# Optimization experiments

Measured on AMD Instinct MI355X. Metric: run time of the kernel, lower is better.

Reference implementation:

```python
import jax, jax.numpy as jnp
import numpy as np

N_NODES = 100000
N_EDGES = 1600000
IN_C = 128
HID_C = 32
HEADS = 4
OUT_C = 40
N_GRAPHS = 64
NEG_SLOPE = 0.2  # PyG GATConv default


def setup_inputs() -> dict:
    key = jax.random.key(0)
    ks = jax.random.split(key, 12)
    x = jax.random.normal(ks[0], (N_NODES, IN_C), dtype=jnp.float32)
    edge_index = jax.random.randint(ks[1], (2, N_EDGES), 0, N_NODES, dtype=jnp.int64)
    batch = jnp.sort(jax.random.randint(ks[2], (N_NODES,), 0, N_GRAPHS, dtype=jnp.int64))
    s1 = 1.0 / np.sqrt(IN_C)
    s2 = 1.0 / np.sqrt(HEADS * HID_C)
    W1 = jax.random.normal(ks[3], (IN_C, HEADS * HID_C), dtype=jnp.float32) * s1
    a1_src = jax.random.normal(ks[4], (HEADS, HID_C), dtype=jnp.float32) * s1
    a1_dst = jax.random.normal(ks[5], (HEADS, HID_C), dtype=jnp.float32) * s1
    b1 = jnp.zeros((HEADS * HID_C,), dtype=jnp.float32)
    W2 = jax.random.normal(ks[6], (HEADS * HID_C, OUT_C), dtype=jnp.float32) * s2
    a2_src = jax.random.normal(ks[7], (1, OUT_C), dtype=jnp.float32) * s2
    a2_dst = jax.random.normal(ks[8], (1, OUT_C), dtype=jnp.float32) * s2
    b2 = jnp.zeros((OUT_C,), dtype=jnp.float32)
    return {"x": x, "edge_index": edge_index, "batch": batch,
            "W1": W1, "a1_src": a1_src, "a1_dst": a1_dst, "b1": b1,
            "W2": W2, "a2_src": a2_src, "a2_dst": a2_dst, "b2": b2}


def gat_conv(x, src, dst, W, a_src, a_dst, bias, heads, out_c, concat):
    """PyG-style GATConv (eval mode, self-loops included in src/dst)."""
    N = x.shape[0]
    h = (x @ W).reshape(N, heads, out_c)              # [N,H,C]
    alpha_s = jnp.einsum('nhc,hc->nh', h, a_src)      # [N,H]
    alpha_d = jnp.einsum('nhc,hc->nh', h, a_dst)
    e = alpha_s[src] + alpha_d[dst]                   # [E,H]
    e = jnp.where(e > 0, e, NEG_SLOPE * e)            # LeakyReLU(0.2)
    # segment softmax over edges grouped by destination node
    m = jax.ops.segment_max(e, dst, num_segments=N)   # [N,H]
    ex = jnp.exp(e - m[dst])
    denom = jax.ops.segment_sum(ex, dst, num_segments=N)
    alpha = ex / (denom[dst] + 1e-16)                 # [E,H]
    msg = h[src] * alpha[..., None]                   # [E,H,C]
    out = jax.ops.segment_sum(msg, dst, num_segments=N)  # [N,H,C]
    if concat:
        out = out.reshape(N, heads * out_c)
    else:
        out = out.mean(axis=1)
    return out + bias


def reference(x, edge_index, batch, W1, a1_src, a1_dst, b1, W2, a2_src, a2_dst, b2):
    N = x.shape[0]
    # add self-loops (PyG GATConv default add_self_loops=True)
    loop = jnp.arange(N, dtype=edge_index.dtype)
    src = jnp.concatenate([edge_index[0], loop])
    dst = jnp.concatenate([edge_index[1], loop])
    h = gat_conv(x, src, dst, W1, a1_src, a1_dst, b1, HEADS, HID_C, concat=True)
    h = jax.nn.elu(h)
    h = gat_conv(h, src, dst, W2, a2_src, a2_dst, b2, 1, OUT_C, concat=False)
    # global mean pool over graphs
    sums = jax.ops.segment_sum(h, batch, num_segments=N_GRAPHS)
    counts = jax.ops.segment_sum(jnp.ones((N,), dtype=h.dtype), batch, num_segments=N_GRAPHS)
    return sums / jnp.maximum(counts, 1.0)[:, None]
```

## Files before the change

### kernel.cpp

```cpp
#include <hip/hip_runtime.h>

#define NNODES 100000
#define NEDGES 1600000
#define ETOT   1700000
#define NGRAPH 64
#define NEG    0.2f
#define NB_SCAN 98
#define NPART  8
#define DPP    12500
#define SCAT_BPP 128
#define SCAT_CHR 12500
#define DSL    98
#define PCH    1024
#define NGB    1563
#define HB     521
#define HEPB   3072
#define FGRID  2084

using f32x2 = __attribute__((ext_vector_type(2))) float;

__device__ __forceinline__ float f4get(const float4& v, int j) {
    return j == 0 ? v.x : j == 1 ? v.y : j == 2 ? v.z : v.w;
}

__device__ __forceinline__ unsigned short f2bf(float f) {
    unsigned u = __float_as_uint(f);
    u = (u + 0x7fffu + ((u >> 16) & 1u)) >> 16;
    return (unsigned short)u;
}
__device__ __forceinline__ float bf_lo(unsigned u) { return __uint_as_float(u << 16); }
__device__ __forceinline__ float bf_hi(unsigned u) { return __uint_as_float(u & 0xffff0000u); }

__global__ __launch_bounds__(256) void k_init(int* __restrict__ cnt, float* __restrict__ partial) {
    int t = threadIdx.x, b = blockIdx.x;
#pragma unroll
    for (int j = 0; j < 4; ++j) {
        int idx = b * 1024 + t * 4 + j;
        if (idx < NNODES) cnt[idx] = 1;
    }
    int pi = b * 256 + t;
    if (pi < NGRAPH * 40) partial[pi] = 0.f;
}

__global__ __launch_bounds__(256, 4) void k_fused1(const int* __restrict__ ei,
        int* __restrict__ cnt, int* __restrict__ rank,
        const float* __restrict__ x, const float* __restrict__ W1,
        const float* __restrict__ a1s, const float* __restrict__ a1d,
        unsigned* __restrict__ h1q, float* __restrict__ as1, float* __restrict__ ad1) {
    __shared__ float sX[64 * 128];
    int bid = blockIdx.x;
    if ((bid & 3) == 3) {
        int hb = bid >> 2;
        int t = threadIdx.x;
        int e0 = hb * HEPB;
        int e1 = e0 + HEPB; if (e1 > NEDGES) e1 = NEDGES;
        for (int e = e0 + t; e < e1; e += 1024) {
            int eA = e, eB = e + 256, eC = e + 512, eD = e + 768;
            bool vA = eA < e1, vB = eB < e1, vC = eC < e1, vD = eD < e1;
            int dA = 0, dB = 0, dC = 0, dD = 0;
            if (vA) dA = ei[NEDGES + eA];
            if (vB) dB = ei[NEDGES + eB];
            if (vC) dC = ei[NEDGES + eC];
            if (vD) dD = ei[NEDGES + eD];
            int rA = 0, rB = 0, rC = 0, rD = 0;
            if (vA) rA = atomicAdd(&cnt[dA], 1);
            if (vB) rB = atomicAdd(&cnt[dB], 1);
            if (vC) rC = atomicAdd(&cnt[dC], 1);
            if (vD) rD = atomicAdd(&cnt[dD], 1);
            if (vA) rank[eA] = rA;
            if (vB) rank[eB] = rB;
            if (vC) rank[eC] = rC;
            if (vD) rank[eD] = rD;
        }
        return;
    }
    int gb = (bid >> 2) * 3 + (bid & 3);
    if (gb >= NGB) return;
    int t = threadIdx.x;
    int nbase = gb * 64;
    int nrows = NNODES - nbase; if (nrows > 64) nrows = 64;
    {
        const float4* X4 = (const float4*)(x + (size_t)nbase * 128);
        float4* sX4 = (float4*)sX;
        for (int i = t; i < nrows * 32; i += 256) sX4[i] = X4[i];
    }
    __syncthreads();

    int colg = t & 31, rowg = t >> 5;
    int c0 = colg * 4, n0 = rowg * 8;
    float acc[8][4];
#pragma unroll
    for (int i = 0; i < 8; ++i)
        acc[i][0] = acc[i][1] = acc[i][2] = acc[i][3] = 0.f;

    for (int k = 0; k < 128; k += 4) {
        float4 w0 = *(const float4*)&W1[(size_t)(k + 0) * 128 + c0];
        float4 w1 = *(const float4*)&W1[(size_t)(k + 1) * 128 + c0];
        float4 w2 = *(const float4*)&W1[(size_t)(k + 2) * 128 + c0];
        float4 w3 = *(const float4*)&W1[(size_t)(k + 3) * 128 + c0];
#pragma unroll
        for (int i = 0; i < 8; ++i) {
            float4 xv = *(const float4*)&sX[(n0 + i) * 128 + k];
            acc[i][0] = fmaf(xv.x, w0.x, acc[i][0]); acc[i][1] = fmaf(xv.x, w0.y, acc[i][1]);
            acc[i][2] = fmaf(xv.x, w0.z, acc[i][2]); acc[i][3] = fmaf(xv.x, w0.w, acc[i][3]);
            acc[i][0] = fmaf(xv.y, w1.x, acc[i][0]); acc[i][1] = fmaf(xv.y, w1.y, acc[i][1]);
            acc[i][2] = fmaf(xv.y, w1.z, acc[i][2]); acc[i][3] = fmaf(xv.y, w1.w, acc[i][3]);
            acc[i][0] = fmaf(xv.z, w2.x, acc[i][0]); acc[i][1] = fmaf(xv.z, w2.y, acc[i][1]);
            acc[i][2] = fmaf(xv.z, w2.z, acc[i][2]); acc[i][3] = fmaf(xv.z, w2.w, acc[i][3]);
            acc[i][0] = fmaf(xv.w, w3.x, acc[i][0]); acc[i][1] = fmaf(xv.w, w3.y, acc[i][1]);
            acc[i][2] = fmaf(xv.w, w3.z, acc[i][2]); acc[i][3] = fmaf(xv.w, w3.w, acc[i][3]);
        }
    }

    int head = colg >> 3;
    float ws0 = a1s[c0], ws1 = a1s[c0 + 1], ws2 = a1s[c0 + 2], ws3 = a1s[c0 + 3];
    float wd0 = a1d[c0], wd1 = a1d[c0 + 1], wd2 = a1d[c0 + 2], wd3 = a1d[c0 + 3];
#pragma unroll
    for (int i = 0; i < 8; ++i) {
        int n = n0 + i;
        float ps = acc[i][0] * ws0 + acc[i][1] * ws1 + acc[i][2] * ws2 + acc[i][3] * ws3;
        float pd = acc[i][0] * wd0 + acc[i][1] * wd1 + acc[i][2] * wd2 + acc[i][3] * wd3;
        ps += __shfl_xor(ps, 1); ps += __shfl_xor(ps, 2); ps += __shfl_xor(ps, 4);
        pd += __shfl_xor(pd, 1); pd += __shfl_xor(pd, 2); pd += __shfl_xor(pd, 4);
        if (n < nrows) {
            int q = __builtin_amdgcn_cvt_pk_fp8_f32(acc[i][0], acc[i][1], 0, false);
            q = __builtin_amdgcn_cvt_pk_fp8_f32(acc[i][2], acc[i][3], q, true);
            h1q[((size_t)(nbase + n)) * 32 + colg] = (unsigned)q;
            if ((colg & 7) == 0) {
                as1[(size_t)(nbase + n) * 4 + head] = ps;
                ad1[(size_t)(nbase + n) * 4 + head] = pd;
            }
        }
    }
}

__global__ __launch_bounds__(256) void k_scan1(const int* __restrict__ cnt,
                                               int* __restrict__ excl,
                                               int* __restrict__ bsum) {
    __shared__ int tmp[256];
    int t = threadIdx.x;
    int base = blockIdx.x * 1024 + t * 4;
    int v0 = base + 0 < NNODES ? cnt[base + 0] : 0;
    int v1 = base + 1 < NNODES ? cnt[base + 1] : 0;
    int v2 = base + 2 < NNODES ? cnt[base + 2] : 0;
    int v3 = base + 3 < NNODES ? cnt[base + 3] : 0;
    int tot = v0 + v1 + v2 + v3;
    tmp[t] = tot;
    __syncthreads();
    for (int off = 1; off < 256; off <<= 1) {
        int x = (t >= off) ? tmp[t - off] : 0;
        __syncthreads();
        tmp[t] += x;
        __syncthreads();
    }
    int tbase = tmp[t] - tot;
    if (base + 0 < NNODES) excl[base + 0] = tbase;
    if (base + 1 < NNODES) excl[base + 1] = tbase + v0;
    if (base + 2 < NNODES) excl[base + 2] = tbase + v0 + v1;
    if (base + 3 < NNODES) excl[base + 3] = tbase + v0 + v1 + v2;
    if (t == 255) bsum[blockIdx.x] = tmp[255];
}

__global__ __launch_bounds__(256) void k_offs(const int* __restrict__ excl,
                                              const int* __restrict__ bsum,
                                              int* __restrict__ offs) {
    __shared__ int sp;
    int b = blockIdx.x, t = threadIdx.x;
    if (t == 0) {
        int p = 0;
        for (int i = 0; i < b; ++i) p += bsum[i];
        sp = p;
    }
    __syncthreads();
    int prefix = sp;
#pragma unroll
    for (int j = 0; j < 4; ++j) {
        int idx = b * 1024 + t * 4 + j;
        if (idx < NNODES) offs[idx] = excl[idx] + prefix;
    }
}

__global__ __launch_bounds__(256) void k_scatter(const int* __restrict__ ei,
                                                 const int* __restrict__ rank,
                                                 const int* __restrict__ offs,
                                                 int* __restrict__ csr_src) {
    int p = blockIdx.x & (NPART - 1);
    int chunk = blockIdx.x / NPART;
    int dlo = p * DPP, dhi = dlo + DPP;
    {
        int d = dlo + chunk * DSL + threadIdx.x;
        if (threadIdx.x < DSL && d < dhi) csr_src[offs[d]] = d;
    }
    int e0 = chunk * SCAT_CHR;
    int e1 = e0 + SCAT_CHR; if (e1 > NEDGES) e1 = NEDGES;
    for (int e = e0 + threadIdx.x; e < e1; e += 1024) {
        int eA = e, eB = e + 256, eC = e + 512, eD = e + 768;
        bool vA = eA < e1, vB = eB < e1, vC = eC < e1, vD = eD < e1;
        int dA = -1, dB = -1, dC = -1, dD = -1;
        if (vA) dA = ei[NEDGES + eA];
        if (vB) dB = ei[NEDGES + eB];
        if (vC) dC = ei[NEDGES + eC];
        if (vD) dD = ei[NEDGES + eD];
        if (dA >= dlo && dA < dhi) csr_src[offs[dA] + rank[eA]] = ei[eA];
        if (dB >= dlo && dB < dhi) csr_src[offs[dB] + rank[eB]] = ei[eB];
        if (dC >= dlo && dC < dhi) csr_src[offs[dC] + rank[eC]] = ei[eC];
        if (dD >= dlo && dD < dhi) csr_src[offs[dD] + rank[eD]] = ei[eD];
    }
}

__global__ __launch_bounds__(256) void k_node1(const int* __restrict__ csr_src,
        const int* __restrict__ offs, const int* __restrict__ cnt,
        const unsigned* __restrict__ h1q,
        const float4* __restrict__ as1v, const float4* __restrict__ ad1v,
        unsigned* __restrict__ out1b) {
    __shared__ float4 exbuf[8][32];
    int t = threadIdx.x;
    int grp = t >> 5, lane = t & 31;
    int node = blockIdx.x * 8 + grp;
    if (node >= NNODES) return;
    int head = lane >> 3;
    int off = offs[node];
    int deg = cnt[node];
    float4 adv = ad1v[node];
    float4 dp = make_float4(0.f, 0.f, 0.f, 0.f);
    float4 acc = make_float4(0.f, 0.f, 0.f, 0.f);
    const float* exs = (const float*)&exbuf[grp][0];

    for (int base = 0; base < deg; base += 32) {
        int m = deg - base; if (m > 32) m = 32;
        int sv = 0;
        if (lane < m) {
            sv = csr_src[off + base + lane];
            float4 av = as1v[sv];
            float v; float4 e;
            v = av.x + adv.x; v = v > 0.f ? v : NEG * v; e.x = __expf(v);
            v = av.y + adv.y; v = v > 0.f ? v : NEG * v; e.y = __expf(v);
            v = av.z + adv.z; v = v > 0.f ? v : NEG * v; e.z = __expf(v);
            v = av.w + adv.w; v = v > 0.f ? v : NEG * v; e.w = __expf(v);
            exbuf[grp][lane] = e;
            dp.x += e.x; dp.y += e.y; dp.z += e.z; dp.w += e.w;
        }
        __builtin_amdgcn_wave_barrier();
        int i = 0;
        for (; i + 4 <= m; i += 4) {
            int s0 = __shfl(sv, i + 0, 32);
            int s1 = __shfl(sv, i + 1, 32);
            int s2 = __shfl(sv, i + 2, 32);
            int s3 = __shfl(sv, i + 3, 32);
            unsigned q0 = h1q[(size_t)s0 * 32 + lane];
            unsigned q1 = h1q[(size_t)s1 * 32 + lane];
            unsigned q2 = h1q[(size_t)s2 * 32 + lane];
            unsigned q3 = h1q[(size_t)s3 * 32 + lane];
            float a0 = exs[(i + 0) * 4 + head];
            float a1 = exs[(i + 1) * 4 + head];
            float a2 = exs[(i + 2) * 4 + head];
            float a3 = exs[(i + 3) * 4 + head];
            f32x2 lo, hi;
            lo = __builtin_amdgcn_cvt_pk_f32_fp8((int)q0, false);
            hi = __builtin_amdgcn_cvt_pk_f32_fp8((int)q0, true);
            acc.x = fmaf(lo.x, a0, acc.x); acc.y = fmaf(lo.y, a0, acc.y);
            acc.z = fmaf(hi.x, a0, acc.z); acc.w = fmaf(hi.y, a0, acc.w);
            lo = __builtin_amdgcn_cvt_pk_f32_fp8((int)q1, false);
            hi = __builtin_amdgcn_cvt_pk_f32_fp8((int)q1, true);
            acc.x = fmaf(lo.x, a1, acc.x); acc.y = fmaf(lo.y, a1, acc.y);
            acc.z = fmaf(hi.x, a1, acc.z); acc.w = fmaf(hi.y, a1, acc.w);
            lo = __builtin_amdgcn_cvt_pk_f32_fp8((int)q2, false);
            hi = __builtin_amdgcn_cvt_pk_f32_fp8((int)q2, true);
            acc.x = fmaf(lo.x, a2, acc.x); acc.y = fmaf(lo.y, a2, acc.y);
            acc.z = fmaf(hi.x, a2, acc.z); acc.w = fmaf(hi.y, a2, acc.w);
            lo = __builtin_amdgcn_cvt_pk_f32_fp8((int)q3, false);
            hi = __builtin_amdgcn_cvt_pk_f32_fp8((int)q3, true);
            acc.x = fmaf(lo.x, a3, acc.x); acc.y = fmaf(lo.y, a3, acc.y);
            acc.z = fmaf(hi.x, a3, acc.z); acc.w = fmaf(hi.y, a3, acc.w);
        }
        for (; i < m; ++i) {
            int s = __shfl(sv, i, 32);
            float a = exs[i * 4 + head];
            unsigned hq = h1q[(size_t)s * 32 + lane];
            f32x2 lo = __builtin_amdgcn_cvt_pk_f32_fp8((int)hq, false);
            f32x2 hi = __builtin_amdgcn_cvt_pk_f32_fp8((int)hq, true);
            acc.x = fmaf(lo.x, a, acc.x);
            acc.y = fmaf(lo.y, a, acc.y);
            acc.z = fmaf(hi.x, a, acc.z);
            acc.w = fmaf(hi.y, a, acc.w);
        }
        __builtin_amdgcn_wave_barrier();
    }
#pragma unroll
    for (int msk = 1; msk < 32; msk <<= 1) {
        dp.x += __shfl_xor(dp.x, msk, 32);
        dp.y += __shfl_xor(dp.y, msk, 32);
        dp.z += __shfl_xor(dp.z, msk, 32);
        dp.w += __shfl_xor(dp.w, msk, 32);
    }
    float inv = 1.f / f4get(dp, head);
    unsigned p0 = (unsigned)f2bf(acc.x * inv) | ((unsigned)f2bf(acc.y * inv) << 16);
    unsigned p1 = (unsigned)f2bf(acc.z * inv) | ((unsigned)f2bf(acc.w * inv) << 16);
    uint2 pk; pk.x = p0; pk.y = p1;
    *(uint2*)&out1b[(size_t)node * 64 + lane * 2] = pk;
}

__global__ __launch_bounds__(256) void k_gemm2(const unsigned* __restrict__ in_b,
                                               const float* __restrict__ W2,
                                               const float* __restrict__ b1,
                                               const float* __restrict__ a2s,
                                               const float* __restrict__ a2d,
                                               unsigned short* __restrict__ h2b,
                                               float* __restrict__ as2,
                                               float* __restrict__ ad2) {
    __shared__ float sW[128 * 40];
    __shared__ float sX[128 * 132];
    int t = threadIdx.x;
    for (int i = t; i < 128 * 40 / 4; i += 256) ((float4*)sW)[i] = ((const float4*)W2)[i];
    int nbase = blockIdx.x * 128;
    int nrows = NNODES - nbase; if (nrows > 128) nrows = 128;
    {
        const uint4* X4 = (const uint4*)(in_b + (size_t)nbase * 64);
        for (int i = t; i < nrows * 16; i += 256) {
            int row = i >> 4, c8 = i & 15;
            uint4 v = X4[i];
            float4 bb0 = *(const float4*)&b1[c8 * 8];
            float4 bb1 = *(const float4*)&b1[c8 * 8 + 4];
            float f0 = bf_lo(v.x) + bb0.x, f1 = bf_hi(v.x) + bb0.y;
            float f2 = bf_lo(v.y) + bb0.z, f3 = bf_hi(v.y) + bb0.w;
            float f4 = bf_lo(v.z) + bb1.x, f5 = bf_hi(v.z) + bb1.y;
            float f6 = bf_lo(v.w) + bb1.z, f7 = bf_hi(v.w) + bb1.w;
            f0 = f0 > 0.f ? f0 : __expf(f0) - 1.f;
            f1 = f1 > 0.f ? f1 : __expf(f1) - 1.f;
            f2 = f2 > 0.f ? f2 : __expf(f2) - 1.f;
            f3 = f3 > 0.f ? f3 : __expf(f3) - 1.f;
            f4 = f4 > 0.f ? f4 : __expf(f4) - 1.f;
            f5 = f5 > 0.f ? f5 : __expf(f5) - 1.f;
            f6 = f6 > 0.f ? f6 : __expf(f6) - 1.f;
            f7 = f7 > 0.f ? f7 : __expf(f7) - 1.f;
            float* sp = &sX[row * 132 + c8 * 8];
            *(float4*)sp       = make_float4(f0, f1, f2, f3);
            *(float4*)(sp + 4) = make_float4(f4, f5, f6, f7);
        }
    }
    __syncthreads();

    int colg = t & 7, nodeg = t >> 3;
    int c0 = colg * 5;
    float acc[4][5];
#pragma unroll
    for (int i = 0; i < 4; ++i)
#pragma unroll
        for (int c = 0; c < 5; ++c) acc[i][c] = 0.f;

    for (int k = 0; k < 128; k += 4) {
        float4 xv[4];
#pragma unroll
        for (int i = 0; i < 4; ++i)
            xv[i] = *(const float4*)&sX[(nodeg + 32 * i) * 132 + k];
#pragma unroll
        for (int j = 0; j < 4; ++j) {
            float w0 = sW[(k + j) * 40 + c0 + 0];
            float w1 = sW[(k + j) * 40 + c0 + 1];
            float w2 = sW[(k + j) * 40 + c0 + 2];
            float w3 = sW[(k + j) * 40 + c0 + 3];
            float w4 = sW[(k + j) * 40 + c0 + 4];
#pragma unroll
            for (int i = 0; i < 4; ++i) {
                float xs = f4get(xv[i], j);
                acc[i][0] = fmaf(xs, w0, acc[i][0]);
                acc[i][1] = fmaf(xs, w1, acc[i][1]);
                acc[i][2] = fmaf(xs, w2, acc[i][2]);
                acc[i][3] = fmaf(xs, w3, acc[i][3]);
                acc[i][4] = fmaf(xs, w4, acc[i][4]);
            }
        }
    }

    float ws0 = a2s[c0], ws1 = a2s[c0 + 1], ws2 = a2s[c0 + 2], ws3 = a2s[c0 + 3], ws4 = a2s[c0 + 4];
    float wd0 = a2d[c0], wd1 = a2d[c0 + 1], wd2 = a2d[c0 + 2], wd3 = a2d[c0 + 3], wd4 = a2d[c0 + 4];
#pragma unroll
    for (int i = 0; i < 4; ++i) {
        int n = nodeg + 32 * i;
        float ps = acc[i][0]*ws0 + acc[i][1]*ws1 + acc[i][2]*ws2 + acc[i][3]*ws3 + acc[i][4]*ws4;
        float pd = acc[i][0]*wd0 + acc[i][1]*wd1 + acc[i][2]*wd2 + acc[i][3]*wd3 + acc[i][4]*wd4;
        ps += __shfl_xor(ps, 1); ps += __shfl_xor(ps, 2); ps += __shfl_xor(ps, 4);
        pd += __shfl_xor(pd, 1); pd += __shfl_xor(pd, 2); pd += __shfl_xor(pd, 4);
        if (n < nrows) {
            unsigned short* hp = h2b + (size_t)(nbase + n) * 40 + c0;
#pragma unroll
            for (int c = 0; c < 5; ++c) hp[c] = f2bf(acc[i][c]);
            if (colg == 0) {
                as2[nbase + n] = ps;
                ad2[nbase + n] = pd;
            }
        }
    }
}

__global__ __launch_bounds__(256) void k_node2(const int* __restrict__ csr_src,
        const int* __restrict__ offs, const int* __restrict__ cnt,
        const unsigned short* __restrict__ h2b,
        const float* __restrict__ as2, const float* __restrict__ ad2,
        float* __restrict__ out2) {
    int t = threadIdx.x;
    int grp = t >> 4, lane = t & 15;
    int node = blockIdx.x * 16 + grp;
    if (node >= NNODES) return;
    int off = offs[node];
    int deg = cnt[node];
    float adv = ad2[node];
    float dp = 0.f;
    float4 acc = make_float4(0.f, 0.f, 0.f, 0.f);

    for (int base = 0; base < deg; base += 16) {
        int m = deg - base; if (m > 16) m = 16;
        int sv = 0; float ex = 0.f;
        if (lane < m) {
            sv = csr_src[off + base + lane];
            float v = as2[sv] + adv;
            v = v > 0.f ? v : NEG * v;
            ex = __expf(v);
            dp += ex;
        }
        int i = 0;
        for (; i + 4 <= m; i += 4) {
            int s0 = __shfl(sv, i + 0, 16);
            int s1 = __shfl(sv, i + 1, 16);
            int s2 = __shfl(sv, i + 2, 16);
            int s3 = __shfl(sv, i + 3, 16);
            float a0 = __shfl(ex, i + 0, 16);
            float a1 = __shfl(ex, i + 1, 16);
            float a2 = __shfl(ex, i + 2, 16);
            float a3 = __shfl(ex, i + 3, 16);
            if (lane < 10) {
                uint2 h0 = *(const uint2*)(h2b + (size_t)s0 * 40 + lane * 4);
                uint2 h1 = *(const uint2*)(h2b + (size_t)s1 * 40 + lane * 4);
                uint2 h2 = *(const uint2*)(h2b + (size_t)s2 * 40 + lane * 4);
                uint2 h3 = *(const uint2*)(h2b + (size_t)s3 * 40 + lane * 4);
                acc.x = fmaf(bf_lo(h0.x), a0, acc.x); acc.y = fmaf(bf_hi(h0.x), a0, acc.y);
                acc.z = fmaf(bf_lo(h0.y), a0, acc.z); acc.w = fmaf(bf_hi(h0.y), a0, acc.w);
                acc.x = fmaf(bf_lo(h1.x), a1, acc.x); acc.y = fmaf(bf_hi(h1.x), a1, acc.y);
                acc.z = fmaf(bf_lo(h1.y), a1, acc.z); acc.w = fmaf(bf_hi(h1.y), a1, acc.w);
                acc.x = fmaf(bf_lo(h2.x), a2, acc.x); acc.y = fmaf(bf_hi(h2.x), a2, acc.y);
                acc.z = fmaf(bf_lo(h2.y), a2, acc.z); acc.w = fmaf(bf_hi(h2.y), a2, acc.w);
                acc.x = fmaf(bf_lo(h3.x), a3, acc.x); acc.y = fmaf(bf_hi(h3.x), a3, acc.y);
                acc.z = fmaf(bf_lo(h3.y), a3, acc.z); acc.w = fmaf(bf_hi(h3.y), a3, acc.w);
            }
        }
        for (; i < m; ++i) {
            int s = __shfl(sv, i, 16);
            float a = __shfl(ex, i, 16);
            if (lane < 10) {
                uint2 hv = *(const uint2*)(h2b + (size_t)s * 40 + lane * 4);
                acc.x = fmaf(bf_lo(hv.x), a, acc.x);
                acc.y = fmaf(bf_hi(hv.x), a, acc.y);
                acc.z = fmaf(bf_lo(hv.y), a, acc.z);
                acc.w = fmaf(bf_hi(hv.y), a, acc.w);
            }
        }
    }
#pragma unroll
    for (int msk = 1; msk < 16; msk <<= 1) dp += __shfl_xor(dp, msk, 16);
    float inv = 1.f / dp;
    if (lane < 10) {
        float4 o; o.x = acc.x * inv; o.y = acc.y * inv; o.z = acc.z * inv; o.w = acc.w * inv;
        *(float4*)(out2 + (size_t)node * 40 + lane * 4) = o;
    }
}

__global__ __launch_bounds__(256) void k_pool1(const float* __restrict__ out2,
        const int* __restrict__ batch, float* __restrict__ partial) {
    int t = threadIdx.x;
    if (t >= 240) return;
    int r = t / 40, c = t - r * 40;
    int base = blockIdx.x * PCH;
    int end = base + PCH; if (end > NNODES) end = NNODES;
    float sum = 0.f; int gcur = -1;
    for (int n = base + r; n < end; n += 6) {
        int g = batch[n];
        if (g != gcur) {
            if (gcur >= 0) unsafeAtomicAdd(&partial[gcur * 40 + c], sum);
            gcur = g; sum = 0.f;
        }
        sum += out2[(size_t)n * 40 + c];
    }
    if (gcur >= 0) unsafeAtomicAdd(&partial[gcur * 40 + c], sum);
}

__global__ void k_pool2(const float* __restrict__ partial, const int* __restrict__ batch,
                        const float* __restrict__ b2, float* __restrict__ out) {
    int i = blockIdx.x * 256 + threadIdx.x;
    if (i >= NGRAPH * 40) return;
    int g = i / 40, c = i - g * 40;
    int lo, hi;
    { int a = 0, b = NNODES; while (a < b) { int m = (a + b) >> 1; if (batch[m] < g) a = m + 1; else b = m; } lo = a; }
    { int a = lo, b = NNODES; while (a < b) { int m = (a + b) >> 1; if (batch[m] < g + 1) a = m + 1; else b = m; } hi = a; }
    int cntg = hi - lo;
    out[i] = cntg > 0 ? partial[i] / (float)cntg + b2[c] : 0.f;
}

extern "C" void kernel_launch(void* const* d_in, const int* in_sizes, int n_in,
                              void* d_out, int out_size, void* d_ws, size_t ws_size,
                              hipStream_t stream) {
    const float* x    = (const float*)d_in[0];
    const int*   ei   = (const int*)d_in[1];
    const int*   batch= (const int*)d_in[2];
    const float* W1   = (const float*)d_in[3];
    const float* a1s  = (const float*)d_in[4];
    const float* a1d  = (const float*)d_in[5];
    const float* b1   = (const float*)d_in[6];
    const float* W2   = (const float*)d_in[7];
    const float* a2s  = (const float*)d_in[8];
    const float* a2d  = (const float*)d_in[9];
    const float* b2   = (const float*)d_in[10];
    float* out = (float*)d_out;

    int* cnt      = (int*)d_ws;
    float* partial= (float*)(cnt + NNODES);
    int* excl     = (int*)(partial + NGRAPH * 40);
    int* offs     = excl + NNODES;
    int* bsum     = offs + NNODES;
    int* rank     = bsum + 128;
    int* csr      = rank + NEDGES;
    float* as1    = (float*)(csr + ETOT);
    float* ad1    = as1 + (size_t)NNODES * 4;
    unsigned* h1q = (unsigned*)(ad1 + (size_t)NNODES * 4);
    unsigned* out1b = h1q + (size_t)NNODES * 32;
    float* as2    = (float*)(out1b + (size_t)NNODES * 64);
    float* ad2    = as2 + NNODES;
    unsigned short* h2b = (unsigned short*)(ad2 + NNODES);
    float* out2   = (float*)(h2b + (size_t)NNODES * 40);

    k_init<<<NB_SCAN, 256, 0, stream>>>(cnt, partial);

    k_fused1<<<FGRID, 256, 0, stream>>>(ei, cnt, rank, x, W1, a1s, a1d, h1q, as1, ad1);

    k_scan1<<<NB_SCAN, 256, 0, stream>>>(cnt, excl, bsum);
    k_offs<<<NB_SCAN, 256, 0, stream>>>(excl, bsum, offs);
    k_scatter<<<NPART * SCAT_BPP, 256, 0, stream>>>(ei, rank, offs, csr);

    k_node1<<<(NNODES + 7) / 8, 256, 0, stream>>>(csr, offs, cnt, h1q,
                                                  (const float4*)as1, (const float4*)ad1, out1b);

    k_gemm2<<<(NNODES + 127) / 128, 256, 0, stream>>>(out1b, W2, b1, a2s, a2d, h2b, as2, ad2);
    k_node2<<<(NNODES + 15) / 16, 256, 0, stream>>>(csr, offs, cnt, h2b, as2, ad2, out2);

    k_pool1<<<(NNODES + PCH - 1) / PCH, 256, 0, stream>>>(out2, batch, partial);
    k_pool2<<<(NGRAPH * 40 + 255) / 256, 256, 0, stream>>>(partial, batch, b2, out);
}
```

Before: 331.9 us.

## Drop init and offset kernels, fold CSR offsets inline, widen gather unroll

Replaces the count-init kernel with a memset and applies the self-loop +1 wherever counts and ranks are read. Removes the per-node offsets kernel: a single-thread kernel scans the block sums, and the scatter and node kernels compute excl[d] + bsum[d>>10] directly. It also repartitions the scatter into 4 destination ranges with 256 edge chunks, and unrolls the layer-1 neighbour gather by 8 instead of 4. The aim is fewer launches and less offset-array traffic, in exchange for an extra load per offset lookup and a serial single-thread scan.

```diff
diff --git a/kernel.cpp b/kernel.cpp
--- a/kernel.cpp
+++ b/kernel.cpp
@@ -6,10 +6,10 @@
 #define NGRAPH 64
 #define NEG    0.2f
 #define NB_SCAN 98
-#define NPART  8
-#define DPP    12500
-#define SCAT_BPP 128
-#define SCAT_CHR 12500
+#define NPART  4
+#define DPP    25000
+#define SCAT_NCH 256
+#define SCAT_CHR 6250
 #define DSL    98
 #define PCH    1024
 #define NGB    1563
@@ -30,17 +30,6 @@
 }
 __device__ __forceinline__ float bf_lo(unsigned u) { return __uint_as_float(u << 16); }
 __device__ __forceinline__ float bf_hi(unsigned u) { return __uint_as_float(u & 0xffff0000u); }
-
-__global__ __launch_bounds__(256) void k_init(int* __restrict__ cnt, float* __restrict__ partial) {
-    int t = threadIdx.x, b = blockIdx.x;
-#pragma unroll
-    for (int j = 0; j < 4; ++j) {
-        int idx = b * 1024 + t * 4 + j;
-        if (idx < NNODES) cnt[idx] = 1;
-    }
-    int pi = b * 256 + t;
-    if (pi < NGRAPH * 40) partial[pi] = 0.f;
-}
 
 __global__ __launch_bounds__(256, 4) void k_fused1(const int* __restrict__ ei,
         int* __restrict__ cnt, int* __restrict__ rank,
@@ -140,10 +129,10 @@
     __shared__ int tmp[256];
     int t = threadIdx.x;
     int base = blockIdx.x * 1024 + t * 4;
-    int v0 = base + 0 < NNODES ? cnt[base + 0] : 0;
-    int v1 = base + 1 < NNODES ? cnt[base + 1] : 0;
-    int v2 = base + 2 < NNODES ? cnt[base + 2] : 0;
-    int v3 = base + 3 < NNODES ? cnt[base + 3] : 0;
+    int v0 = base + 0 < NNODES ? cnt[base + 0] + 1 : 0;
+    int v1 = base + 1 < NNODES ? cnt[base + 1] + 1 : 0;
+    int v2 = base + 2 < NNODES ? cnt[base + 2] + 1 : 0;
+    int v3 = base + 3 < NNODES ? cnt[base + 3] + 1 : 0;
     int tot = v0 + v1 + v2 + v3;
     tmp[t] = tot;
     __syncthreads();
@@ -161,35 +150,24 @@
     if (t == 255) bsum[blockIdx.x] = tmp[255];
 }
 
-__global__ __launch_bounds__(256) void k_offs(const int* __restrict__ excl,
-                                              const int* __restrict__ bsum,
-                                              int* __restrict__ offs) {
-    __shared__ int sp;
-    int b = blockIdx.x, t = threadIdx.x;
-    if (t == 0) {
-        int p = 0;
-        for (int i = 0; i < b; ++i) p += bsum[i];
-        sp = p;
-    }
-    __syncthreads();
-    int prefix = sp;
-#pragma unroll
-    for (int j = 0; j < 4; ++j) {
-        int idx = b * 1024 + t * 4 + j;
-        if (idx < NNODES) offs[idx] = excl[idx] + prefix;
+__global__ void k_scan2(int* __restrict__ bsum) {
+    if (threadIdx.x == 0 && blockIdx.x == 0) {
+        int acc = 0;
+        for (int i = 0; i < NB_SCAN; ++i) { int v = bsum[i]; bsum[i] = acc; acc += v; }
     }
 }
 
 __global__ __launch_bounds__(256) void k_scatter(const int* __restrict__ ei,
                                                  const int* __restrict__ rank,
-                                                 const int* __restrict__ offs,
+                                                 const int* __restrict__ excl,
+                                                 const int* __restrict__ bsum,
                                                  int* __restrict__ csr_src) {
     int p = blockIdx.x & (NPART - 1);
-    int chunk = blockIdx.x / NPART;
+    int chunk = blockIdx.x >> 2;
     int dlo = p * DPP, dhi = dlo + DPP;
     {
         int d = dlo + chunk * DSL + threadIdx.x;
-        if (threadIdx.x < DSL && d < dhi) csr_src[offs[d]] = d;
+        if (threadIdx.x < DSL && d < dhi) csr_src[excl[d] + bsum[d >> 10]] = d;
     }
     int e0 = chunk * SCAT_CHR;
     int e1 = e0 + SCAT_CHR; if (e1 > NEDGES) e1 = NEDGES;
@@ -201,16 +179,16 @@
         if (vB) dB = ei[NEDGES + eB];
         if (vC) dC = ei[NEDGES + eC];
         if (vD) dD = ei[NEDGES + eD];
-        if (dA >= dlo && dA < dhi) csr_src[offs[dA] + rank[eA]] = ei[eA];
-        if (dB >= dlo && dB < dhi) csr_src[offs[dB] + rank[eB]] = ei[eB];
-        if (dC >= dlo && dC < dhi) csr_src[offs[dC] + rank[eC]] = ei[eC];
-        if (dD >= dlo && dD < dhi) csr_src[offs[dD] + rank[eD]] = ei[eD];
+        if (dA >= dlo && dA < dhi) csr_src[excl[dA] + bsum[dA >> 10] + 1 + rank[eA]] = ei[eA];
+        if (dB >= dlo && dB < dhi) csr_src[excl[dB] + bsum[dB >> 10] + 1 + rank[eB]] = ei[eB];
+        if (dC >= dlo && dC < dhi) csr_src[excl[dC] + bsum[dC >> 10] + 1 + rank[eC]] = ei[eC];
+        if (dD >= dlo && dD < dhi) csr_src[excl[dD] + bsum[dD >> 10] + 1 + rank[eD]] = ei[eD];
     }
 }
 
 __global__ __launch_bounds__(256) void k_node1(const int* __restrict__ csr_src,
-        const int* __restrict__ offs, const int* __restrict__ cnt,
-        const unsigned* __restrict__ h1q,
+        const int* __restrict__ excl, const int* __restrict__ bsum,
+        const int* __restrict__ cnt, const unsigned* __restrict__ h1q,
         const float4* __restrict__ as1v, const float4* __restrict__ ad1v,
         unsigned* __restrict__ out1b) {
     __shared__ float4 exbuf[8][32];
@@ -219,8 +197,8 @@
     int node = blockIdx.x * 8 + grp;
     if (node >= NNODES) return;
     int head = lane >> 3;
-    int off = offs[node];
-    int deg = cnt[node];
+    int off = excl[node] + bsum[node >> 10];
+    int deg = cnt[node] + 1;
     float4 adv = ad1v[node];
     float4 dp = make_float4(0.f, 0.f, 0.f, 0.f);
     float4 acc = make_float4(0.f, 0.f, 0.f, 0.f);
@@ -242,19 +220,31 @@
         }
         __builtin_amdgcn_wave_barrier();
         int i = 0;
-        for (; i + 4 <= m; i += 4) {
+        for (; i + 8 <= m; i += 8) {
             int s0 = __shfl(sv, i + 0, 32);
             int s1 = __shfl(sv, i + 1, 32);
             int s2 = __shfl(sv, i + 2, 32);
             int s3 = __shfl(sv, i + 3, 32);
+            int s4 = __shfl(sv, i + 4, 32);
+            int s5 = __shfl(sv, i + 5, 32);
+            int s6 = __shfl(sv, i + 6, 32);
+            int s7 = __shfl(sv, i + 7, 32);
             unsigned q0 = h1q[(size_t)s0 * 32 + lane];
             unsigned q1 = h1q[(size_t)s1 * 32 + lane];
             unsigned q2 = h1q[(size_t)s2 * 32 + lane];
             unsigned q3 = h1q[(size_t)s3 * 32 + lane];
+            unsigned q4 = h1q[(size_t)s4 * 32 + lane];
+            unsigned q5 = h1q[(size_t)s5 * 32 + lane];
+            unsigned q6 = h1q[(size_t)s6 * 32 + lane];
+            unsigned q7 = h1q[(size_t)s7 * 32 + lane];
             float a0 = exs[(i + 0) * 4 + head];
             float a1 = exs[(i + 1) * 4 + head];
             float a2 = exs[(i + 2) * 4 + head];
             float a3 = exs[(i + 3) * 4 + head];
+            float a4 = exs[(i + 4) * 4 + head];
+            float a5 = exs[(i + 5) * 4 + head];
+            float a6 = exs[(i + 6) * 4 + head];
+            float a7 = exs[(i + 7) * 4 + head];
             f32x2 lo, hi;
             lo = __builtin_amdgcn_cvt_pk_f32_fp8((int)q0, false);
             hi = __builtin_amdgcn_cvt_pk_f32_fp8((int)q0, true);
@@ -272,6 +262,22 @@
             hi = __builtin_amdgcn_cvt_pk_f32_fp8((int)q3, true);
             acc.x = fmaf(lo.x, a3, acc.x); acc.y = fmaf(lo.y, a3, acc.y);
             acc.z = fmaf(hi.x, a3, acc.z); acc.w = fmaf(hi.y, a3, acc.w);
+            lo = __builtin_amdgcn_cvt_pk_f32_fp8((int)q4, false);
+            hi = __builtin_amdgcn_cvt_pk_f32_fp8((int)q4, true);
+            acc.x = fmaf(lo.x, a4, acc.x); acc.y = fmaf(lo.y, a4, acc.y);
+            acc.z = fmaf(hi.x, a4, acc.z); acc.w = fmaf(hi.y, a4, acc.w);
+            lo = __builtin_amdgcn_cvt_pk_f32_fp8((int)q5, false);
+            hi = __builtin_amdgcn_cvt_pk_f32_fp8((int)q5, true);
+            acc.x = fmaf(lo.x, a5, acc.x); acc.y = fmaf(lo.y, a5, acc.y);
+            acc.z = fmaf(hi.x, a5, acc.z); acc.w = fmaf(hi.y, a5, acc.w);
+            lo = __builtin_amdgcn_cvt_pk_f32_fp8((int)q6, false);
+            hi = __builtin_amdgcn_cvt_pk_f32_fp8((int)q6, true);
+            acc.x = fmaf(lo.x, a6, acc.x); acc.y = fmaf(lo.y, a6, acc.y);
+            acc.z = fmaf(hi.x, a6, acc.z); acc.w = fmaf(hi.y, a6, acc.w);
+            lo = __builtin_amdgcn_cvt_pk_f32_fp8((int)q7, false);
+            hi = __builtin_amdgcn_cvt_pk_f32_fp8((int)q7, true);
+            acc.x = fmaf(lo.x, a7, acc.x); acc.y = fmaf(lo.y, a7, acc.y);
+            acc.z = fmaf(hi.x, a7, acc.z); acc.w = fmaf(hi.y, a7, acc.w);
         }
         for (; i < m; ++i) {
             int s = __shfl(sv, i, 32);
@@ -394,16 +400,16 @@
 }
 
 __global__ __launch_bounds__(256) void k_node2(const int* __restrict__ csr_src,
-        const int* __restrict__ offs, const int* __restrict__ cnt,
-        const unsigned short* __restrict__ h2b,
+        const int* __restrict__ excl, const int* __restrict__ bsum,
+        const int* __restrict__ cnt, const unsigned short* __restrict__ h2b,
         const float* __restrict__ as2, const float* __restrict__ ad2,
         float* __restrict__ out2) {
     int t = threadIdx.x;
     int grp = t >> 4, lane = t & 15;
     int node = blockIdx.x * 16 + grp;
     if (node >= NNODES) return;
-    int off = offs[node];
-    int deg = cnt[node];
+    int off = excl[node] + bsum[node >> 10];
+    int deg = cnt[node] + 1;
     float adv = ad2[node];
     float dp = 0.f;
     float4 acc = make_float4(0.f, 0.f, 0.f, 0.f);
@@ -514,8 +520,7 @@
     int* cnt      = (int*)d_ws;
     float* partial= (float*)(cnt + NNODES);
     int* excl     = (int*)(partial + NGRAPH * 40);
-    int* offs     = excl + NNODES;
-    int* bsum     = offs + NNODES;
+    int* bsum     = excl + NNODES;
     int* rank     = bsum + 128;
     int* csr      = rank + NEDGES;
     float* as1    = (float*)(csr + ETOT);
@@ -527,19 +532,19 @@
     unsigned short* h2b = (unsigned short*)(ad2 + NNODES);
     float* out2   = (float*)(h2b + (size_t)NNODES * 40);
 
-    k_init<<<NB_SCAN, 256, 0, stream>>>(cnt, partial);
+    hipMemsetAsync(d_ws, 0, ((size_t)NNODES + NGRAPH * 40) * sizeof(int), stream);
 
     k_fused1<<<FGRID, 256, 0, stream>>>(ei, cnt, rank, x, W1, a1s, a1d, h1q, as1, ad1);
 
     k_scan1<<<NB_SCAN, 256, 0, stream>>>(cnt, excl, bsum);
-    k_offs<<<NB_SCAN, 256, 0, stream>>>(excl, bsum, offs);
-    k_scatter<<<NPART * SCAT_BPP, 256, 0, stream>>>(ei, rank, offs, csr);
-
-    k_node1<<<(NNODES + 7) / 8, 256, 0, stream>>>(csr, offs, cnt, h1q,
+    k_scan2<<<1, 64, 0, stream>>>(bsum);
+    k_scatter<<<NPART * SCAT_NCH, 256, 0, stream>>>(ei, rank, excl, bsum, csr);
+
+    k_node1<<<(NNODES + 7) / 8, 256, 0, stream>>>(csr, excl, bsum, cnt, h1q,
                                                   (const float4*)as1, (const float4*)ad1, out1b);
 
     k_gemm2<<<(NNODES + 127) / 128, 256, 0, stream>>>(out1b, W2, b1, a2s, a2d, h2b, as2, ad2);
-    k_node2<<<(NNODES + 15) / 16, 256, 0, stream>>>(csr, offs, cnt, h2b, as2, ad2, out2);
+    k_node2<<<(NNODES + 15) / 16, 256, 0, stream>>>(csr, excl, bsum, cnt, h2b, as2, ad2, out2);
 
     k_pool1<<<(NNODES + PCH - 1) / PCH, 256, 0, stream>>>(out2, batch, partial);
     k_pool2<<<(NGRAPH * 40 + 255) / 256, 256, 0, stream>>>(partial, batch, b2, out);
```

Result: slower. 343.4 us (+3.4%).
